# Optimization experiments

Measured on AMD Instinct MI355X. Metric: run time of the kernel, lower is better.

Reference implementation:

```python
import jax, jax.numpy as jnp
import numpy as np

B, S, HID, NH = 4, 2048, 512, 8
DH = HID // NH
NEG = -1000000.0


def setup_inputs() -> dict:
    key = jax.random.key(0)
    ks = jax.random.split(key, 8)
    scale = 1.0 / np.sqrt(HID)
    return {
        "queries": jax.random.normal(ks[0], (B, S, HID), dtype=jnp.float32),
        "keys": jax.random.normal(ks[1], (B, S, HID), dtype=jnp.float32),
        "values": jax.random.normal(ks[2], (B, S, HID), dtype=jnp.float32),
        "valid_lens": jax.random.randint(ks[3], (B,), 1, S + 1, dtype=jnp.int32),
        "Wq": jax.random.uniform(ks[4], (HID, HID), jnp.float32, -scale, scale),
        "Wk": jax.random.uniform(ks[5], (HID, HID), jnp.float32, -scale, scale),
        "Wv": jax.random.uniform(ks[6], (HID, HID), jnp.float32, -scale, scale),
        "Wo": jax.random.uniform(ks[7], (HID, HID), jnp.float32, -scale, scale),
    }


def _split_heads(x):
    # (B, S, HID) -> (B, NH, S, DH)
    return x.reshape(B, S, NH, DH).transpose(0, 2, 1, 3)


def reference(queries, keys, values, valid_lens, Wq, Wk, Wv, Wo):
    q = _split_heads(queries @ Wq.T)
    k = _split_heads(keys @ Wk.T)
    v = _split_heads(values @ Wv.T)
    scores = jnp.einsum("bhqd,bhkd->bhqk", q, k) / jnp.sqrt(jnp.float32(DH))
    # valid_lens is per-batch; mask key positions >= valid_len with -1e6 (as in sequence_mask)
    mask = jnp.arange(S)[None, :] < valid_lens[:, None]          # (B, S)
    scores = jnp.where(mask[:, None, None, :], scores, NEG)
    attn = jax.nn.softmax(scores, axis=-1)
    out = jnp.einsum("bhqk,bhkd->bhqd", attn, v)                 # (B, NH, S, DH)
    out = out.transpose(0, 2, 1, 3).reshape(B, S, HID)
    return out @ Wo.T
```

## Files before the change

kernel.cpp:

```cpp
#include <hip/hip_runtime.h>

#define B_ 4
#define S_ 2048
#define HIDN 512
#define NH 8
#define DH 64

typedef __attribute__((ext_vector_type(8))) short short8;
typedef __attribute__((ext_vector_type(4))) short short4v;
typedef __attribute__((ext_vector_type(8))) __bf16 bf16x8;
typedef __attribute__((ext_vector_type(4))) float floatx4;
typedef __attribute__((ext_vector_type(2))) unsigned uint2v;
typedef __attribute__((ext_vector_type(4))) unsigned uint4v;

__device__ inline short f2bf(float f) {
    union { float f; unsigned u; } x; x.f = f;
    unsigned r = x.u + 0x7fffu + ((x.u >> 16) & 1u);
    return (short)(r >> 16);
}

__device__ inline unsigned pack2(float a, float b) {
    unsigned ua = __builtin_bit_cast(unsigned, a) + 0x8000u;
    unsigned ub = __builtin_bit_cast(unsigned, b) + 0x8000u;
    return __builtin_amdgcn_perm(ub, ua, 0x07060302);
}

__device__ inline short8 cvt8(const float* __restrict__ p) {
    floatx4 f0 = *(const floatx4*)p;
    floatx4 f1 = *(const floatx4*)(p + 4);
    uint4v u;
    u[0] = pack2(f0[0], f0[1]); u[1] = pack2(f0[2], f0[3]);
    u[2] = pack2(f1[0], f1[1]); u[3] = pack2(f1[2], f1[3]);
    return __builtin_bit_cast(short8, u);
}

__device__ inline floatx4 mfma_s(short8 a, short8 b, floatx4 c) {
    return __builtin_amdgcn_mfma_f32_16x16x32_bf16(
        __builtin_bit_cast(bf16x8, a), __builtin_bit_cast(bf16x8, b), c, 0, 0, 0);
}

__device__ inline float vmax4(floatx4 v) {
    return fmaxf(fmaxf(v[0], v[1]), fmaxf(v[2], v[3]));
}

__global__ void cvt_w(const float* __restrict__ wq, const float* __restrict__ wk,
                      const float* __restrict__ wv, short* __restrict__ out) {
    const float* src = blockIdx.y == 0 ? wq : (blockIdx.y == 1 ? wk : wv);
    int i = (blockIdx.x * 256 + threadIdx.x) * 4;
    floatx4 f = *(const floatx4*)&src[i];
    short4v v; v[0]=f2bf(f[0]); v[1]=f2bf(f[1]); v[2]=f2bf(f[2]); v[3]=f2bf(f[3]);
    *(short4v*)&out[blockIdx.y * (HIDN * HIDN) + i] = v;
}

__global__ __launch_bounds__(256) void gemm_qkv(const float* __restrict__ xq,
                                                const float* __restrict__ xk,
                                                const float* __restrict__ xv,
                                                const short* __restrict__ wb,
                                                short* __restrict__ Qh,
                                                short* __restrict__ Kh,
                                                short* __restrict__ VT) {
    const int z = blockIdx.z;
    const float* X = z == 0 ? xq : (z == 1 ? xk : xv);
    const short* W = wb + z * (HIDN * HIDN);
    short* dstQK = z == 0 ? Qh : Kh;

    __shared__ __align__(16) short Als[128][72];
    __shared__ __align__(16) short Bls[128][72];

    const int t = threadIdx.x;
    const int w = t >> 6, lane = t & 63, quad = lane >> 4, l16 = lane & 15;
    const int wm = (w & 1) * 64, wn = (w >> 1) * 64;
    const int m0 = blockIdx.x * 128, n0 = blockIdx.y * 128;

    floatx4 acc[4][4];
    floatx4 zero = {0.f, 0.f, 0.f, 0.f};
#pragma unroll
    for (int i = 0; i < 4; i++)
#pragma unroll
        for (int j = 0; j < 4; j++) acc[i][j] = zero;

    const int row0 = t >> 3;
    const int c8 = (t & 7) * 8;

    for (int k0 = 0; k0 < HIDN; k0 += 64) {
        __syncthreads();
#pragma unroll
        for (int rr = 0; rr < 4; rr++)
            *(short8*)&Als[row0 + rr*32][c8] =
                cvt8(&X[(m0 + row0 + rr*32) * HIDN + k0 + c8]);
#pragma unroll
        for (int rr = 0; rr < 4; rr++)
            *(short8*)&Bls[row0 + rr*32][c8] =
                *(const short8*)&W[(n0 + row0 + rr*32) * HIDN + k0 + c8];
        __syncthreads();

#pragma unroll
        for (int ks = 0; ks < 2; ks++) {
            const int cq8 = (ks * 4 + quad) * 8;
            short8 a[4], b[4];
#pragma unroll
            for (int i = 0; i < 4; i++)
                a[i] = *(const short8*)&Als[wm + i*16 + l16][cq8];
#pragma unroll
            for (int j = 0; j < 4; j++)
                b[j] = *(const short8*)&Bls[wn + j*16 + l16][cq8];
#pragma unroll
            for (int i = 0; i < 4; i++)
#pragma unroll
                for (int j = 0; j < 4; j++)
                    acc[i][j] = mfma_s(a[i], b[j], acc[i][j]);
        }
    }

    if (z < 2) {
#pragma unroll
        for (int i = 0; i < 4; i++)
#pragma unroll
            for (int j = 0; j < 4; j++)
#pragma unroll
                for (int r = 0; r < 4; r++) {
                    int m = m0 + wm + i*16 + quad*4 + r;
                    int n = n0 + wn + j*16 + l16;
                    int bb = m >> 11, s = m & 2047, h = n >> 6, d = n & 63;
                    dstQK[((bb * NH + h) * S_ + s) * DH + d] = f2bf(acc[i][j][r]);
                }
    } else {
#pragma unroll
        for (int i = 0; i < 4; i++)
#pragma unroll
            for (int j = 0; j < 4; j++) {
                int s0 = m0 + wm + i*16 + quad*4;
                int n = n0 + wn + j*16 + l16;
                int bb = s0 >> 11, s = s0 & 2047, h = n >> 6, d = n & 63;
                uint2v v;
                v[0] = pack2(acc[i][j][0], acc[i][j][1]);
                v[1] = pack2(acc[i][j][2], acc[i][j][3]);
                *(uint2v*)&VT[((bb * NH + h) * DH + d) * S_ + s] = v;
            }
    }
}

__global__ __launch_bounds__(256) void gemm_out(const short* __restrict__ AO,
                                                const float* __restrict__ Wo,
                                                float* __restrict__ C) {
    __shared__ __align__(16) short Als[128][72];
    __shared__ __align__(16) short Bls[64][72];

    const int t = threadIdx.x;
    const int w = t >> 6, lane = t & 63, quad = lane >> 4, l16 = lane & 15;
    const int wm = (w & 1) * 64, wn = (w >> 1) * 32;
    const int m0 = blockIdx.x * 128, n0 = blockIdx.y * 64;

    floatx4 acc[4][2];
    floatx4 zero = {0.f, 0.f, 0.f, 0.f};
#pragma unroll
    for (int i = 0; i < 4; i++)
#pragma unroll
        for (int j = 0; j < 2; j++) acc[i][j] = zero;

    const int row0 = t >> 3;
    const int c8 = (t & 7) * 8;

    for (int k0 = 0; k0 < HIDN; k0 += 64) {
        __syncthreads();
#pragma unroll
        for (int rr = 0; rr < 4; rr++)
            *(short8*)&Als[row0 + rr*32][c8] =
                *(const short8*)&AO[(m0 + row0 + rr*32) * HIDN + k0 + c8];
#pragma unroll
        for (int rr = 0; rr < 2; rr++)
            *(short8*)&Bls[row0 + rr*32][c8] =
                cvt8(&Wo[(n0 + row0 + rr*32) * HIDN + k0 + c8]);
        __syncthreads();

#pragma unroll
        for (int ks = 0; ks < 2; ks++) {
            const int cq8 = (ks * 4 + quad) * 8;
            short8 a[4], b[2];
#pragma unroll
            for (int i = 0; i < 4; i++)
                a[i] = *(const short8*)&Als[wm + i*16 + l16][cq8];
#pragma unroll
            for (int j = 0; j < 2; j++)
                b[j] = *(const short8*)&Bls[wn + j*16 + l16][cq8];
#pragma unroll
            for (int i = 0; i < 4; i++)
#pragma unroll
                for (int j = 0; j < 2; j++)
                    acc[i][j] = mfma_s(a[i], b[j], acc[i][j]);
        }
    }

#pragma unroll
    for (int i = 0; i < 4; i++)
#pragma unroll
        for (int j = 0; j < 2; j++)
#pragma unroll
            for (int r = 0; r < 4; r++) {
                int m = m0 + wm + i*16 + quad*4 + r;
                int n = n0 + wn + j*16 + l16;
                C[m * HIDN + n] = acc[i][j][r];
            }
}

__global__ __launch_bounds__(256, 4) void attn_kernel(const short* __restrict__ Qh,
                                                      const short* __restrict__ Kh,
                                                      const short* __restrict__ VT,
                                                      const int* __restrict__ vlen,
                                                      short* __restrict__ AO) {
    __shared__ __align__(16) short Ksh[128 * 64];
    __shared__ __align__(16) short Vsh[64 * 128];
    short* Psh = Ksh;

    const int t = threadIdx.x, w = t >> 6, lane = t & 63;
    const int quad = lane >> 4, l16 = lane & 15;
    const int qb = blockIdx.x * 64;
    const int h = blockIdx.y, b = blockIdx.z;
    const int bh = b * NH + h;
    const int vl = vlen[b];
    const int nt = (vl + 127) >> 7;

    const float SC = 0.180336879f;

    const short* qrow = &Qh[(bh * S_ + qb + w * 16 + l16) * DH];
    short8 qa0 = *(const short8*)&qrow[quad * 8];
    short8 qa1 = *(const short8*)&qrow[32 + quad * 8];

    const int krow = t >> 3;
    const int kc = t & 7;
    const int vd = t >> 4;
    const int vc = t & 15;
    int kgo[4], klo[4], vgo[4], vlo[4];
#pragma unroll
    for (int it = 0; it < 4; it++) {
        const int kr_ = krow + it * 32;
        kgo[it] = kr_ * DH + (kc << 3);
        klo[it] = kr_ * 64 + ((kc ^ (kr_ & 7)) << 3);
        const int vd_ = vd + it * 16;
        vgo[it] = vd_ * S_ + (vc << 3);
        vlo[it] = vd_ * 128 + ((vc ^ (vd_ & 7)) << 3);
    }

    const short* Kgb = &Kh[(size_t)bh * S_ * DH];
    const short* Vgb = &VT[(size_t)bh * DH * S_];

    short8 krg[4], vrg[4];
#pragma unroll
    for (int it = 0; it < 4; it++) krg[it] = *(const short8*)&Kgb[kgo[it]];
#pragma unroll
    for (int it = 0; it < 4; it++) vrg[it] = *(const short8*)&Vgb[vgo[it]];

    float m_run = -1e30f, l_run = 0.f;
    floatx4 Oacc[4];
    floatx4 zero = {0.f, 0.f, 0.f, 0.f};
#pragma unroll
    for (int dt = 0; dt < 4; dt++) Oacc[dt] = zero;

    for (int kt = 0; kt < nt; kt++) {
        const int base = kt << 7;
        const bool bnd = (base + 128) > vl;

        __syncthreads();
#pragma unroll
        for (int it = 0; it < 4; it++) *(short8*)&Ksh[klo[it]] = krg[it];
#pragma unroll
        for (int it = 0; it < 4; it++) *(short8*)&Vsh[vlo[it]] = vrg[it];
        __syncthreads();

        if (kt + 1 < nt) {
            const int nb = (kt + 1) << 7;
#pragma unroll
            for (int it = 0; it < 4; it++)
                krg[it] = *(const short8*)&Kgb[nb * DH + kgo[it]];
#pragma unroll
            for (int it = 0; it < 4; it++)
                vrg[it] = *(const short8*)&Vgb[nb + vgo[it]];
        }

        floatx4 sc[8];
#pragma unroll
        for (int n = 0; n < 8; n++) {
            int kro = n * 16 + l16;
            const short* kr = &Ksh[kro * 64];
            short8 kb0 = *(const short8*)&kr[((quad ^ (kro & 7)) << 3)];
            short8 kb1 = *(const short8*)&kr[(((4 + quad) ^ (kro & 7)) << 3)];
            floatx4 s = zero;
            s = mfma_s(kb0, qa0, s);
            s = mfma_s(kb1, qa1, s);
            sc[n] = s;
        }
        __syncthreads();

        if (bnd) {
#pragma unroll
            for (int n = 0; n < 8; n++)
#pragma unroll
                for (int r = 0; r < 4; r++) {
                    int key = base + n * 16 + quad * 4 + r;
                    if (key >= vl) sc[n][r] = -1e30f;
                }
        }

        float mx = vmax4(sc[0]);
#pragma unroll
        for (int n = 1; n < 8; n++) mx = fmaxf(mx, vmax4(sc[n]));
        mx = fmaxf(mx, __shfl_xor(mx, 16));
        mx = fmaxf(mx, __shfl_xor(mx, 32));
        const float mxs = mx * SC;
        const bool norescale = __all(mxs <= m_run);
        const float mnew = norescale ? m_run : fmaxf(m_run, mxs);
        const float alpha = norescale ? 1.0f : __builtin_amdgcn_exp2f(m_run - mnew);
        m_run = mnew;
        float rs = 0.f;
#pragma unroll
        for (int n = 0; n < 8; n++)
#pragma unroll
            for (int r = 0; r < 4; r++) {
                float p = __builtin_amdgcn_exp2f(fmaf(sc[n][r], SC, -mnew));
                sc[n][r] = p;
                rs += p;
            }
        rs += __shfl_xor(rs, 16);
        rs += __shfl_xor(rs, 32);
        l_run = l_run * alpha + rs;
        if (!norescale) {
#pragma unroll
            for (int dt = 0; dt < 4; dt++)
#pragma unroll
                for (int r = 0; r < 4; r++) Oacc[dt][r] *= alpha;
        }

#pragma unroll
        for (int n = 0; n < 8; n++) {
            unsigned lo = pack2(sc[n][0], sc[n][1]);
            unsigned hi = pack2(sc[n][2], sc[n][3]);
            int c = (n << 1) + (quad >> 1);
            int idx = (w << 11) + (l16 << 7) + ((c ^ (l16 & 7)) << 3) + ((quad & 1) << 2);
            uint2v pv; pv[0] = lo; pv[1] = hi;
            *(uint2v*)&Psh[idx] = pv;
        }
        asm volatile("s_waitcnt lgkmcnt(0)" ::: "memory");
        __builtin_amdgcn_sched_barrier(0);

#pragma unroll
        for (int kk = 0; kk < 4; kk++) {
            int pc = (kk << 2) + quad;
            short8 pf = *(const short8*)&Psh[(w << 11) + (l16 << 7) + ((pc ^ (l16 & 7)) << 3)];
#pragma unroll
            for (int dt = 0; dt < 4; dt++) {
                int vrow = dt * 16 + l16;
                short8 vf = *(const short8*)&Vsh[vrow * 128 + ((pc ^ (vrow & 7)) << 3)];
                Oacc[dt] = mfma_s(vf, pf, Oacc[dt]);
            }
        }
    }

    float inv = 1.0f / l_run;
    int q = qb + w * 16 + l16;
    short* dst = &AO[(b * S_ + q) * HIDN + h * DH];
#pragma unroll
    for (int dt = 0; dt < 4; dt++) {
        uint2v v;
        v[0] = pack2(Oacc[dt][0] * inv, Oacc[dt][1] * inv);
        v[1] = pack2(Oacc[dt][2] * inv, Oacc[dt][3] * inv);
        *(uint2v*)&dst[dt * 16 + quad * 4] = v;
    }
}

extern "C" void kernel_launch(void* const* d_in, const int* in_sizes, int n_in,
                              void* d_out, int out_size, void* d_ws, size_t ws_size,
                              hipStream_t stream) {
    const float* q  = (const float*)d_in[0];
    const float* k  = (const float*)d_in[1];
    const float* v  = (const float*)d_in[2];
    const int*   vl = (const int*)d_in[3];
    const float* wq = (const float*)d_in[4];
    const float* wk = (const float*)d_in[5];
    const float* wv = (const float*)d_in[6];
    const float* wo = (const float*)d_in[7];
    float* out = (float*)d_out;

    const size_t HSZ = (size_t)B_ * NH * S_ * DH;
    short* Qh  = (short*)d_ws;
    short* Kh  = Qh + HSZ;
    short* VT  = Kh + HSZ;
    short* AO  = VT + HSZ;
    short* Wqkv = AO;

    dim3 blk(256);
    cvt_w<<<dim3(256, 3), blk, 0, stream>>>(wq, wk, wv, Wqkv);
    gemm_qkv<<<dim3(64, 4, 3), blk, 0, stream>>>(q, k, v, Wqkv, Qh, Kh, VT);
    attn_kernel<<<dim3(S_ / 64, NH, B_), blk, 0, stream>>>(Qh, Kh, VT, vl, AO);
    gemm_out<<<dim3(64, 8), blk, 0, stream>>>(AO, wo, out);
}
```

Baseline: 184.5 us.

## Double-buffer K/V tiles in LDS using direct global-to-LDS loads

The attention kernel now stages K and V tiles straight from global memory into LDS with global_load_lds, into two ping-pong buffers. The next tile is prefetched while the current one is computed, which removes the register staging, the LDS store pass and one barrier per iteration. The XOR swizzle moves from the LDS address to the global source address. Shared memory per block doubles, so the occupancy hint drops from 4 to 2 blocks per CU. Correctness depends on the barrier at the top of the loop also waiting for the outstanding async LDS writes.

```diff
diff --git a/kernel.cpp b/kernel.cpp
--- a/kernel.cpp
+++ b/kernel.cpp
@@ -41,6 +41,12 @@
 
 __device__ inline float vmax4(floatx4 v) {
     return fmaxf(fmaxf(v[0], v[1]), fmaxf(v[2], v[3]));
+}
+
+__device__ inline void gl_lds(const short* g, short* l) {
+    __builtin_amdgcn_global_load_lds(
+        (const __attribute__((address_space(1))) void*)g,
+        (__attribute__((address_space(3))) void*)l, 16, 0, 0);
 }
 
 __global__ void cvt_w(const float* __restrict__ wq, const float* __restrict__ wk,
@@ -203,14 +209,13 @@
             }
 }
 
-__global__ __launch_bounds__(256, 4) void attn_kernel(const short* __restrict__ Qh,
+__global__ __launch_bounds__(256, 2) void attn_kernel(const short* __restrict__ Qh,
                                                       const short* __restrict__ Kh,
                                                       const short* __restrict__ VT,
                                                       const int* __restrict__ vlen,
                                                       short* __restrict__ AO) {
-    __shared__ __align__(16) short Ksh[128 * 64];
-    __shared__ __align__(16) short Vsh[64 * 128];
-    short* Psh = Ksh;
+    __shared__ __align__(16) short Ksh[2][128 * 64];
+    __shared__ __align__(16) short Vsh[2][64 * 128];
 
     const int t = threadIdx.x, w = t >> 6, lane = t & 63;
     const int quad = lane >> 4, l16 = lane & 15;
@@ -226,29 +231,33 @@
     short8 qa0 = *(const short8*)&qrow[quad * 8];
     short8 qa1 = *(const short8*)&qrow[32 + quad * 8];
 
-    const int krow = t >> 3;
-    const int kc = t & 7;
-    const int vd = t >> 4;
-    const int vc = t & 15;
-    int kgo[4], klo[4], vgo[4], vlo[4];
+    int kgo[4], vgo[4];
 #pragma unroll
     for (int it = 0; it < 4; it++) {
-        const int kr_ = krow + it * 32;
-        kgo[it] = kr_ * DH + (kc << 3);
-        klo[it] = kr_ * 64 + ((kc ^ (kr_ & 7)) << 3);
-        const int vd_ = vd + it * 16;
-        vgo[it] = vd_ * S_ + (vc << 3);
-        vlo[it] = vd_ * 128 + ((vc ^ (vd_ & 7)) << 3);
-    }
+        int idx = it * 256 + t;
+        int row = idx >> 3, c = idx & 7;
+        kgo[it] = row * DH + ((c ^ (row & 7)) << 3);
+        int d = idx >> 4, cv = idx & 15;
+        vgo[it] = d * S_ + ((cv ^ (d & 7)) << 3);
+    }
+    const int ldsb = (t & ~63) * 8;
 
     const short* Kgb = &Kh[(size_t)bh * S_ * DH];
     const short* Vgb = &VT[(size_t)bh * DH * S_];
 
-    short8 krg[4], vrg[4];
-#pragma unroll
-    for (int it = 0; it < 4; it++) krg[it] = *(const short8*)&Kgb[kgo[it]];
-#pragma unroll
-    for (int it = 0; it < 4; it++) vrg[it] = *(const short8*)&Vgb[vgo[it]];
+#define STAGE(bufsel, tb)                                                     \
+    {                                                                         \
+        const short* Kg_ = Kgb + (tb) * DH;                                   \
+        const short* Vg_ = Vgb + (tb);                                        \
+        _Pragma("unroll")                                                     \
+        for (int it = 0; it < 4; it++)                                        \
+            gl_lds(Kg_ + kgo[it], &Ksh[bufsel][it * 2048 + ldsb]);            \
+        _Pragma("unroll")                                                     \
+        for (int it = 0; it < 4; it++)                                        \
+            gl_lds(Vg_ + vgo[it], &Vsh[bufsel][it * 2048 + ldsb]);            \
+    }
+
+    STAGE(0, 0)
 
     float m_run = -1e30f, l_run = 0.f;
     floatx4 Oacc[4];
@@ -259,29 +268,20 @@
     for (int kt = 0; kt < nt; kt++) {
         const int base = kt << 7;
         const bool bnd = (base + 128) > vl;
-
-        __syncthreads();
-#pragma unroll
-        for (int it = 0; it < 4; it++) *(short8*)&Ksh[klo[it]] = krg[it];
-#pragma unroll
-        for (int it = 0; it < 4; it++) *(short8*)&Vsh[vlo[it]] = vrg[it];
-        __syncthreads();
-
-        if (kt + 1 < nt) {
-            const int nb = (kt + 1) << 7;
-#pragma unroll
-            for (int it = 0; it < 4; it++)
-                krg[it] = *(const short8*)&Kgb[nb * DH + kgo[it]];
-#pragma unroll
-            for (int it = 0; it < 4; it++)
-                vrg[it] = *(const short8*)&Vgb[nb + vgo[it]];
-        }
+        const int cur = kt & 1;
+        const short* Kc = Ksh[cur];
+        const short* Vc = Vsh[cur];
+        short* Psh = Ksh[cur];
+
+        __syncthreads();
+
+        if (kt + 1 < nt) STAGE(cur ^ 1, base + 128)
 
         floatx4 sc[8];
 #pragma unroll
         for (int n = 0; n < 8; n++) {
             int kro = n * 16 + l16;
-            const short* kr = &Ksh[kro * 64];
+            const short* kr = &Kc[kro * 64];
             short8 kb0 = *(const short8*)&kr[((quad ^ (kro & 7)) << 3)];
             short8 kb1 = *(const short8*)&kr[(((4 + quad) ^ (kro & 7)) << 3)];
             floatx4 s = zero;
@@ -349,11 +349,12 @@
 #pragma unroll
             for (int dt = 0; dt < 4; dt++) {
                 int vrow = dt * 16 + l16;
-                short8 vf = *(const short8*)&Vsh[vrow * 128 + ((pc ^ (vrow & 7)) << 3)];
+                short8 vf = *(const short8*)&Vc[vrow * 128 + ((pc ^ (vrow & 7)) << 3)];
                 Oacc[dt] = mfma_s(vf, pf, Oacc[dt]);
             }
         }
     }
+#undef STAGE
 
     float inv = 1.0f / l_run;
     int q = qb + w * 16 + l16;
```

Measured after the change: 189.4 us. 1.03x slower.
